# Kernel tuning notes

Hardware: AMD Instinct MI355X
Metric: run time of the kernel (lower is better)

## Reference

```python
import jax, jax.numpy as jnp
import numpy as np

B, L, ENC, D, H, HD, MLP, R = 4, 512, 512, 1024, 16, 64, 4096, 32
NUM_BUCKETS, MAX_DISTANCE = 32, 128
EPS = 1e-6
NEG = -1e10


def rmsnorm(x, scale):
    var = jnp.mean(jnp.square(x), axis=-1, keepdims=True)
    return x * jax.lax.rsqrt(var + EPS) * scale


def rel_pos_bias(table, qlen, klen):
    # T5 causal (bidirectional=False) relative position bucketing.
    ctx = jnp.arange(qlen)[:, None]
    mem = jnp.arange(klen)[None, :]
    rp = mem - ctx                      # [q, k]
    n = -jnp.minimum(rp, 0)             # distance into the past
    max_exact = NUM_BUCKETS // 2
    is_small = n < max_exact
    large = max_exact + (
        jnp.log(jnp.maximum(n, 1).astype(jnp.float32) / max_exact)
        / np.log(MAX_DISTANCE / max_exact) * (NUM_BUCKETS - max_exact)
    ).astype(jnp.int32)
    large = jnp.minimum(large, NUM_BUCKETS - 1)
    bucket = jnp.where(is_small, n, large)
    return table[bucket].transpose(2, 0, 1)[None]  # [1, h, q, k]


def lora_dense(x, W, a, b):
    # x:[B,L,d]  W:[d,e]  a:[B,d,r]  b:[B,r,e]  -> xW + (xa)b per example
    out = jnp.einsum('bld,de->ble', x, W)
    low = jnp.einsum('bld,bdr->blr', x, a)
    return out + jnp.einsum('blr,bre->ble', low, b)


def attention(xq, xkv, Wq, Wk, Wv, Wo, qa, qb, ka, kb, va, vb, oa, ob, bias):
    b, ql, _ = xq.shape
    kl = xkv.shape[1]
    q = lora_dense(xq, Wq, qa, qb).reshape(b, ql, H, HD) * (1.0 / np.sqrt(HD))
    k = lora_dense(xkv, Wk, ka, kb).reshape(b, kl, H, HD)
    v = lora_dense(xkv, Wv, va, vb).reshape(b, kl, H, HD)
    scores = jnp.einsum('bqhd,bkhd->bhqk', q, k)
    if bias is not None:
        scores = scores + bias
    probs = jax.nn.softmax(scores, axis=-1)
    ctx = jnp.einsum('bhqk,bkhd->bqhd', probs, v).reshape(b, ql, H * HD)
    return lora_dense(ctx, Wo, oa, ob)


def setup_inputs() -> dict:
    key = jax.random.key(0)
    ks = jax.random.split(key, 32)
    s = 0.02
    inp = {
        'inputs':  jax.random.normal(ks[0], (B, L, D), jnp.float32),
        'encoded': jax.random.normal(ks[1], (B, ENC, D), jnp.float32),
        'lora_qa': jax.random.normal(ks[2], (B, 2, D, R), jnp.float32) * s,
        'lora_qb': jax.random.normal(ks[3], (B, 2, R, D), jnp.float32) * s,
        'lora_ka': jax.random.normal(ks[4], (B, 2, D, R), jnp.float32) * s,
        'lora_kb': jax.random.normal(ks[5], (B, 2, R, D), jnp.float32) * s,
        'lora_va': jax.random.normal(ks[6], (B, 2, D, R), jnp.float32) * s,
        'lora_vb': jax.random.normal(ks[7], (B, 2, R, D), jnp.float32) * s,
        'lora_oa': jax.random.normal(ks[8], (B, 2, D, R), jnp.float32) * s,
        'lora_ob': jax.random.normal(ks[9], (B, 2, R, D), jnp.float32) * s,
        'rel_table': jax.random.normal(ks[10], (NUM_BUCKETS, H), jnp.float32) * s,
        'ln1': jnp.ones((D,), jnp.float32),
        'ln2': jnp.ones((D,), jnp.float32),
        'ln3': jnp.ones((D,), jnp.float32),
        'sWq': jax.random.normal(ks[11], (D, H * HD), jnp.float32) * s,
        'sWk': jax.random.normal(ks[12], (D, H * HD), jnp.float32) * s,
        'sWv': jax.random.normal(ks[13], (D, H * HD), jnp.float32) * s,
        'sWo': jax.random.normal(ks[14], (H * HD, D), jnp.float32) * s,
        'cWq': jax.random.normal(ks[15], (D, H * HD), jnp.float32) * s,
        'cWk': jax.random.normal(ks[16], (D, H * HD), jnp.float32) * s,
        'cWv': jax.random.normal(ks[17], (D, H * HD), jnp.float32) * s,
        'cWo': jax.random.normal(ks[18], (H * HD, D), jnp.float32) * s,
        'wi0': jax.random.normal(ks[19], (D, MLP), jnp.float32) * s,
        'wi1': jax.random.normal(ks[20], (D, MLP), jnp.float32) * s,
        'wo_mlp': jax.random.normal(ks[21], (MLP, D), jnp.float32) * s,
    }
    return inp


def reference(inputs, encoded, lora_qa, lora_qb, lora_ka, lora_kb, lora_va, lora_vb,
              lora_oa, lora_ob, rel_table, ln1, ln2, ln3,
              sWq, sWk, sWv, sWo, cWq, cWk, cWv, cWo, wi0, wi1, wo_mlp):
    l = inputs.shape[1]
    causal = jnp.tril(jnp.ones((l, l), dtype=bool))
    dec_bias = rel_pos_bias(rel_table, l, l) + jnp.where(causal, 0.0, NEG)[None, None]

    # --- self-attention block ---
    x = rmsnorm(inputs, ln1)
    x = attention(x, x, sWq, sWk, sWv, sWo,
                  lora_qa[:, 0], lora_qb[:, 0], lora_ka[:, 0], lora_kb[:, 0],
                  lora_va[:, 0], lora_vb[:, 0], lora_oa[:, 0], lora_ob[:, 0],
                  dec_bias)
    x = x + inputs

    # --- cross-attention block ---
    y = rmsnorm(x, ln2)
    y = attention(y, encoded, cWq, cWk, cWv, cWo,
                  lora_qa[:, 1], lora_qb[:, 1], lora_ka[:, 1], lora_kb[:, 1],
                  lora_va[:, 1], lora_vb[:, 1], lora_oa[:, 1], lora_ob[:, 1],
                  None)
    y = y + x

    # --- gated-gelu MLP block (T5 v1.1 style) ---
    lz = rmsnorm(y, ln3)
    h = jax.nn.gelu(lz @ wi0, approximate=False) * (lz @ wi1)
    z = h @ wo_mlp + y
    return z
```

## Files before the change

### kernel.cpp

```cpp
#include <hip/hip_runtime.h>
#include <math.h>


#define DEV __device__ __forceinline__

typedef __bf16 bf16x8 __attribute__((ext_vector_type(8)));
typedef float floatx4 __attribute__((ext_vector_type(4)));

typedef __attribute__((address_space(1))) void* gas_ptr;
typedef __attribute__((address_space(3))) void* las_ptr;

DEV unsigned short f2bf(float f) {
  union { float f; unsigned int u; } v; v.f = f;
  unsigned int r = v.u + 0x7fffu + ((v.u >> 16) & 1u);
  return (unsigned short)(r >> 16);
}
DEV float bf2f(unsigned short u) {
  union { unsigned int u; float f; } v; v.u = ((unsigned int)u) << 16;
  return v.f;
}

#define GLOAD_LDS16(g, l) __builtin_amdgcn_global_load_lds((gas_ptr)(g), (las_ptr)(l), 16, 0, 0)

template<int NW>
DEV void stage_tile(const char* gbase, char* lds, int nrows, int ldbytes, int wave, int lane) {
  int nchunks = nrows >> 3;
  for (int c = wave; c < nchunks; c += NW) {
    int row  = (c << 3) + (lane >> 3);
    int colb = (lane & 7) << 4;
    GLOAD_LDS16(gbase + (size_t)row * ldbytes + colb, lds + (c << 10));
  }
}

template<int NW>
DEV void stage_tile_sw(const char* gbase, char* lds, int nrows, int ldbytes, int wave, int lane) {
  int nchunks = nrows >> 3;
  int colb = (((lane & 7) ^ ((lane >> 3) & 7)) << 4);
  for (int c = wave; c < nchunks; c += NW) {
    int row = (c << 3) + (lane >> 3);
    GLOAD_LDS16(gbase + (size_t)row * ldbytes + colb, lds + (c << 10));
  }
}

template<int NW>
DEV void stage_tile256(const char* gbase, char* lds, int nrows, int ldbytes, int wave, int lane) {
  int nchunks = nrows >> 2;
  for (int c = wave; c < nchunks; c += NW) {
    int row  = (c << 2) + (lane >> 4);
    int colb = (lane & 15) << 4;
    GLOAD_LDS16(gbase + (size_t)row * ldbytes + colb, lds + (c << 10));
  }
}

template<int WM, int WN>
DEV void gemm_core(const unsigned short* A, const unsigned short* Bt, float* C,
                   int K, int lda, int ldb, int ldc, int m0, int n0,
                   char* ldsA, char* ldsB) {
  constexpr int NW = WM * WN;
  const int tid  = threadIdx.x;
  const int lane = tid & 63;
  const int wave = tid >> 6;
  const int wm   = wave % WM;
  const int wn   = wave / WM;
  const int quad = lane >> 4;
  const int l15  = lane & 15;
  const int key  = l15 & 7;

  floatx4 acc[4][4];
#pragma unroll
  for (int i = 0; i < 4; ++i)
#pragma unroll
    for (int j = 0; j < 4; ++j) acc[i][j] = (floatx4){0.f, 0.f, 0.f, 0.f};

  const char* gA = (const char*)(A + (size_t)m0 * lda);
  const char* gB = (const char*)(Bt + (size_t)n0 * ldb);

  for (int k0 = 0; k0 < K; k0 += 64) {
    stage_tile_sw<NW>(gA + (size_t)k0 * 2, ldsA, WM * 64, lda * 2, wave, lane);
    stage_tile_sw<NW>(gB + (size_t)k0 * 2, ldsB, WN * 64, ldb * 2, wave, lane);
    __syncthreads();
#pragma unroll
    for (int kk = 0; kk < 64; kk += 32) {
      bf16x8 af[4], bv[4];
      int off = (((kk >> 3) + quad) ^ key) << 4;
      const char* baseA = ldsA + (size_t)(wm * 64 + l15) * 128 + off;
      const char* baseB = ldsB + (size_t)(wn * 64 + l15) * 128 + off;
#pragma unroll
      for (int mi = 0; mi < 4; ++mi) af[mi] = *(const bf16x8*)(baseA + mi * 2048);
#pragma unroll
      for (int ni = 0; ni < 4; ++ni) bv[ni] = *(const bf16x8*)(baseB + ni * 2048);
#pragma unroll
      for (int mi = 0; mi < 4; ++mi)
#pragma unroll
        for (int ni = 0; ni < 4; ++ni)
          acc[mi][ni] = __builtin_amdgcn_mfma_f32_16x16x32_bf16(af[mi], bv[ni], acc[mi][ni], 0, 0, 0);
    }
    __syncthreads();
  }

#pragma unroll
  for (int mi = 0; mi < 4; ++mi) {
#pragma unroll
    for (int r = 0; r < 4; ++r) {
      int row = m0 + wm * 64 + mi * 16 + quad * 4 + r;
#pragma unroll
      for (int ni = 0; ni < 4; ++ni) {
        int col = n0 + wn * 64 + ni * 16 + l15;
        C[(size_t)row * ldc + col] = acc[mi][ni][r];
      }
    }
  }
}

__global__ __launch_bounds__(256) void k_gemm1s(const unsigned short* A, const unsigned short* Bt,
                                                float* Cpart, size_t pstride,
                                                int Kchunk, int lda, int ldb, int ldc) {
  __shared__ char lds[32768];
  int s = blockIdx.z;
  size_t koff = (size_t)s * Kchunk;
  gemm_core<2, 2>(A + koff, Bt + koff, Cpart + (size_t)s * pstride,
                  Kchunk, lda, ldb, ldc,
                  blockIdx.y * 128, blockIdx.x * 128, lds, lds + 16384);
}

struct GXSlice {
  const unsigned short* A0;
  const unsigned short* Aext;
  const unsigned short* B0;
  const unsigned short* Bext;
  float* C;
  size_t bextb;
  int ldc, nxa, it0, it1;
};
struct GX { GXSlice s[4]; };

__global__ __launch_bounds__(256) void k_gemmx(GX g) {
  __shared__ char lds[32768];
  char* ldsA = lds;
  char* ldsB = lds + 16384;
  GXSlice sl = g.s[blockIdx.z];
  if ((int)blockIdx.x >= sl.nxa) return;
  const int m0 = blockIdx.y * 128, n0 = blockIdx.x * 128;
  const int b = m0 >> 9;
  const int tid = threadIdx.x, lane = tid & 63, wave = tid >> 6;
  const int wm = wave & 1, wn = wave >> 1;
  const int quad = lane >> 4, l15 = lane & 15;
  const int key = l15 & 7;

  floatx4 acc[4][4];
#pragma unroll
  for (int i = 0; i < 4; ++i)
#pragma unroll
    for (int j = 0; j < 4; ++j) acc[i][j] = (floatx4){0.f, 0.f, 0.f, 0.f};

  for (int it = sl.it0; it < sl.it1; ++it) {
    if (it < 16) {
      stage_tile_sw<4>((const char*)sl.A0 + (size_t)m0 * 2048 + it * 128, ldsA, 128, 2048, wave, lane);
      stage_tile_sw<4>((const char*)sl.B0 + (size_t)n0 * 2048 + it * 128, ldsB, 128, 2048, wave, lane);
    } else {
      int eb = (it - 16) * 128;
      stage_tile_sw<4>((const char*)sl.Aext + (size_t)m0 * 256 + eb, ldsA, 128, 256, wave, lane);
      stage_tile_sw<4>((const char*)(sl.Bext + (size_t)b * sl.bextb) + (size_t)n0 * 256 + eb,
                       ldsB, 128, 256, wave, lane);
    }
    __syncthreads();
#pragma unroll
    for (int kk = 0; kk < 64; kk += 32) {
      bf16x8 af[4], bv[4];
      int off = (((kk >> 3) + quad) ^ key) << 4;
      const char* baseA = ldsA + (size_t)(wm * 64 + l15) * 128 + off;
      const char* baseB = ldsB + (size_t)(wn * 64 + l15) * 128 + off;
#pragma unroll
      for (int mi = 0; mi < 4; ++mi) af[mi] = *(const bf16x8*)(baseA + mi * 2048);
#pragma unroll
      for (int ni = 0; ni < 4; ++ni) bv[ni] = *(const bf16x8*)(baseB + ni * 2048);
#pragma unroll
      for (int mi = 0; mi < 4; ++mi)
#pragma unroll
        for (int ni = 0; ni < 4; ++ni)
          acc[mi][ni] = __builtin_amdgcn_mfma_f32_16x16x32_bf16(af[mi], bv[ni], acc[mi][ni], 0, 0, 0);
    }
    __syncthreads();
  }

#pragma unroll
  for (int mi = 0; mi < 4; ++mi) {
#pragma unroll
    for (int r = 0; r < 4; ++r) {
      int row = m0 + wm * 64 + mi * 16 + quad * 4 + r;
#pragma unroll
      for (int ni = 0; ni < 4; ++ni) {
        int col = n0 + wn * 64 + ni * 16 + l15;
        sl.C[(size_t)row * sl.ldc + col] = acc[mi][ni][r];
      }
    }
  }
}

__global__ __launch_bounds__(256) void k_qkvsum(const float* bqs, const float* bqc,
                                                unsigned short* qbf, unsigned short* kbf,
                                                unsigned short* kbf2) {
  const size_t PS = (size_t)2048 * 3072, PC = (size_t)2048 * 2048;
  int t = threadIdx.x;
  int row0 = blockIdx.x * 8;
  int zc = blockIdx.y;
  for (int j = 0; j < 8; ++j) {
    int row = row0 + j;
    int nsec = zc ? 1 : 2;
    for (int sec = 0; sec < nsec; ++sec) {
      const float* base = zc ? (bqc + (size_t)row * 2048 + sec * 1024)
                             : (bqs + (size_t)row * 3072 + sec * 1024);
      float4 a = ((const float4*)base)[t];
      float4 c = ((const float4*)(base + (zc ? PC : PS)))[t];
      float4 s; s.x = a.x + c.x; s.y = a.y + c.y; s.z = a.z + c.z; s.w = a.w + c.w;
      ushort4 o; o.x = f2bf(s.x); o.y = f2bf(s.y); o.z = f2bf(s.z); o.w = f2bf(s.w);
      unsigned short* dst = zc ? kbf2 : (sec == 0 ? qbf : kbf);
      ((ushort4*)(dst + (size_t)row * 1024))[t] = o;
    }
  }
}

__global__ __launch_bounds__(256) void k_vtrans2(const float* bqs, const float* bqc,
                                                 unsigned short* vtb, unsigned short* vtb2) {
  __shared__ float tl[64][65];
  int which = blockIdx.z;
  int z = blockIdx.y, b = z >> 4, h = z & 15;
  int k0 = blockIdx.x * 64;
  int ld = which ? 2048 : 3072;
  int voff = which ? 1024 : 2048;
  const float* src = which ? bqc : bqs;
  size_t PARTW = (size_t)2048 * ld;
  unsigned short* dst = which ? vtb2 : vtb;
  int t = threadIdx.x;
  {
    int kr = t >> 2, c0 = (t & 3) * 16;
    const float* p = src + (size_t)(b * 512 + k0 + kr) * ld + voff + h * 64 + c0;
#pragma unroll
    for (int i = 0; i < 4; ++i) {
      float4 v0 = *(const float4*)(p + i * 4);
      float4 v1 = *(const float4*)(p + PARTW + i * 4);
      tl[kr][c0 + i * 4 + 0] = v0.x + v1.x;
      tl[kr][c0 + i * 4 + 1] = v0.y + v1.y;
      tl[kr][c0 + i * 4 + 2] = v0.z + v1.z;
      tl[kr][c0 + i * 4 + 3] = v0.w + v1.w;
    }
  }
  __syncthreads();
  {
    int dw = t >> 2, kc = (t & 3) * 16;
    union { unsigned short us[16]; uint4 q[2]; } pk;
#pragma unroll
    for (int j = 0; j < 16; ++j) pk.us[j] = f2bf(tl[kc + j][dw]);
    uint4* dp = (uint4*)(dst + ((size_t)z * 64 + dw) * 512 + k0 + kc);
    dp[0] = pk.q[0]; dp[1] = pk.q[1];
  }
}

template<bool CAUSAL, bool QSUM>
__global__ __launch_bounds__(256) void k_flash(const unsigned short* qmat, const float* qparts,
                                               const unsigned short* kmat, const unsigned short* vt,
                                               const float* rb, unsigned short* ctxb) {
  __shared__ char ldsQ[8192];
  __shared__ char ldsK[16384];
  __shared__ char ldsV[16384];
  __shared__ char ldsP[16384];
  __shared__ float lrb[512];

  const size_t PART = (size_t)2048 * 1024;
  const int z = blockIdx.y, b = z >> 4, h = z & 15;
  const int q0 = blockIdx.x * 64;
  const int tid = threadIdx.x, lane = tid & 63, wave = tid >> 6;
  const int quad = lane >> 4, l15 = lane & 15;

  const unsigned short* K = kmat + (size_t)b * 512 * 1024 + h * 64;
  const unsigned short* V = vt + (size_t)z * 64 * 512;

  if (QSUM) {
#pragma unroll
    for (int rr = 0; rr < 4; ++rr) {
      int row = rr * 16 + (tid >> 4);
      int c4 = tid & 15;
      const float* src = qparts + (size_t)(q0 + row) * 1024 + h * 64 + c4 * 4;
      float4 s0 = *(const float4*)src;
      float4 s1 = *(const float4*)(src + PART);
      float4 s2 = *(const float4*)(src + 2 * PART);
      float4 s3 = *(const float4*)(src + 3 * PART);
      ushort4 o;
      o.x = f2bf(s0.x + s1.x + s2.x + s3.x);
      o.y = f2bf(s0.y + s1.y + s2.y + s3.y);
      o.z = f2bf(s0.z + s1.z + s2.z + s3.z);
      o.w = f2bf(s0.w + s1.w + s2.w + s3.w);
      *(ushort4*)(ldsQ + (size_t)row * 128 + c4 * 8) = o;
    }
  } else {
    const unsigned short* Q = qmat + (size_t)b * 512 * 1024 + h * 64;
    stage_tile<4>((const char*)(Q + (size_t)q0 * 1024), ldsQ, 64, 2048, wave, lane);
  }
  if (CAUSAL)
    for (int i = tid; i < 512; i += 256) lrb[i] = rb[h * 512 + i];

  float m_run[4], l_run[4];
  floatx4 oacc[4];
#pragma unroll
  for (int r = 0; r < 4; ++r) { m_run[r] = -1e30f; l_run[r] = 0.f; }
#pragma unroll
  for (int ni = 0; ni < 4; ++ni) oacc[ni] = (floatx4){0.f, 0.f, 0.f, 0.f};

  const int ktend = CAUSAL ? (blockIdx.x / 2 + 1) : 4;
  for (int kt = 0; kt < ktend; ++kt) {
    __syncthreads();
    stage_tile<4>((const char*)(K + (size_t)kt * 128 * 1024), ldsK, 128, 2048, wave, lane);
    stage_tile256<4>((const char*)(V + kt * 128), ldsV, 64, 1024, wave, lane);
    __syncthreads();

    floatx4 sacc[8];
#pragma unroll
    for (int ct = 0; ct < 8; ++ct) sacc[ct] = (floatx4){0.f, 0.f, 0.f, 0.f};
    const char* aBase = ldsQ + (size_t)(wave * 16 + l15) * 128 + quad * 16;
#pragma unroll
    for (int kd = 0; kd < 2; ++kd) {
      bf16x8 af = *(const bf16x8*)(aBase + kd * 64);
#pragma unroll
      for (int ct = 0; ct < 8; ++ct) {
        bf16x8 bf = *(const bf16x8*)(ldsK + (size_t)(ct * 16 + l15) * 128 + quad * 16 + kd * 64);
        sacc[ct] = __builtin_amdgcn_mfma_f32_16x16x32_bf16(af, bf, sacc[ct], 0, 0, 0);
      }
    }

    float sv[8][4];
#pragma unroll
    for (int ct = 0; ct < 8; ++ct)
#pragma unroll
      for (int r = 0; r < 4; ++r) {
        float v = sacc[ct][r] * 0.125f;
        if (CAUSAL) {
          int qq = q0 + wave * 16 + quad * 4 + r;
          int kk = kt * 128 + ct * 16 + l15;
          v = (kk <= qq) ? v + lrb[qq - kk] : -1e30f;
        }
        sv[ct][r] = v;
      }

    float mx[4];
#pragma unroll
    for (int r = 0; r < 4; ++r) {
      mx[r] = sv[0][r];
#pragma unroll
      for (int ct = 1; ct < 8; ++ct) mx[r] = fmaxf(mx[r], sv[ct][r]);
    }
#pragma unroll
    for (int o = 1; o < 16; o <<= 1)
#pragma unroll
      for (int r = 0; r < 4; ++r) mx[r] = fmaxf(mx[r], __shfl_xor(mx[r], o));

    float alpha[4], rs[4];
#pragma unroll
    for (int r = 0; r < 4; ++r) {
      float mn = fmaxf(m_run[r], mx[r]);
      alpha[r] = __expf(m_run[r] - mn);
      m_run[r] = mn;
      rs[r] = 0.f;
    }
#pragma unroll
    for (int ct = 0; ct < 8; ++ct)
#pragma unroll
      for (int r = 0; r < 4; ++r) {
        float p = __expf(sv[ct][r] - m_run[r]);
        sv[ct][r] = p;
        rs[r] += p;
      }
#pragma unroll
    for (int o = 1; o < 16; o <<= 1)
#pragma unroll
      for (int r = 0; r < 4; ++r) rs[r] += __shfl_xor(rs[r], o);
#pragma unroll
    for (int r = 0; r < 4; ++r) l_run[r] = l_run[r] * alpha[r] + rs[r];
#pragma unroll
    for (int ni = 0; ni < 4; ++ni)
#pragma unroll
      for (int r = 0; r < 4; ++r) oacc[ni][r] *= alpha[r];

#pragma unroll
    for (int ct = 0; ct < 8; ++ct)
#pragma unroll
      for (int r = 0; r < 4; ++r)
        *(unsigned short*)(ldsP + (size_t)(wave * 16 + quad * 4 + r) * 256 + (ct * 16 + l15) * 2)
            = f2bf(sv[ct][r]);
    __syncthreads();

    const char* pBase = ldsP + (size_t)(wave * 16 + l15) * 256 + quad * 16;
#pragma unroll
    for (int kk = 0; kk < 4; ++kk) {
      bf16x8 pf = *(const bf16x8*)(pBase + kk * 64);
#pragma unroll
      for (int ni = 0; ni < 4; ++ni) {
        bf16x8 vf8 = *(const bf16x8*)(ldsV + (size_t)(ni * 16 + l15) * 256 + quad * 16 + kk * 64);
        oacc[ni] = __builtin_amdgcn_mfma_f32_16x16x32_bf16(pf, vf8, oacc[ni], 0, 0, 0);
      }
    }
  }

#pragma unroll
  for (int r = 0; r < 4; ++r) {
    int q = q0 + wave * 16 + quad * 4 + r;
    float inv = 1.0f / l_run[r];
    unsigned short* dst = ctxb + ((size_t)b * 512 + q) * 1024 + h * 64;
#pragma unroll
    for (int ni = 0; ni < 4; ++ni)
      dst[ni * 16 + l15] = f2bf(oacc[ni][r] * inv);
  }
}

__global__ __launch_bounds__(512) void k_mlp(const unsigned short* A, const unsigned short* Wc,
                                             unsigned short* hbf) {
  __shared__ char lds[49152];
  char* ldsA = lds;
  char* ldsB = lds + 16384;
  const int m0 = blockIdx.y * 128;
  const int n0 = blockIdx.x * 128;
  const int tid = threadIdx.x, lane = tid & 63, wave = tid >> 6;
  const int half = wave >> 2, wl = wave & 3;
  const int wm = wl & 1, wn = wl >> 1;
  const int quad = lane >> 4, l15 = lane & 15;
  const int key = l15 & 7;

  floatx4 acc[4][4];
#pragma unroll
  for (int i = 0; i < 4; ++i)
#pragma unroll
    for (int j = 0; j < 4; ++j) acc[i][j] = (floatx4){0.f, 0.f, 0.f, 0.f};

  const char* gA = (const char*)(A + (size_t)m0 * 1024);
  const char* gB = (const char*)(Wc + (size_t)blockIdx.x * 256 * 1024);

  for (int k0 = 0; k0 < 1024; k0 += 64) {
    stage_tile_sw<8>(gA + (size_t)k0 * 2, ldsA, 128, 2048, wave, lane);
    stage_tile_sw<8>(gB + (size_t)k0 * 2, ldsB, 256, 2048, wave, lane);
    __syncthreads();
#pragma unroll
    for (int kk = 0; kk < 64; kk += 32) {
      bf16x8 af[4], bv[4];
      int off = (((kk >> 3) + quad) ^ key) << 4;
      const char* baseA = ldsA + (size_t)(wm * 64 + l15) * 128 + off;
      const char* baseB = ldsB + (size_t)(half * 128 + wn * 64 + l15) * 128 + off;
#pragma unroll
      for (int mi = 0; mi < 4; ++mi) af[mi] = *(const bf16x8*)(baseA + mi * 2048);
#pragma unroll
      for (int ni = 0; ni < 4; ++ni) bv[ni] = *(const bf16x8*)(baseB + ni * 2048);
#pragma unroll
      for (int mi = 0; mi < 4; ++mi)
#pragma unroll
        for (int ni = 0; ni < 4; ++ni)
          acc[mi][ni] = __builtin_amdgcn_mfma_f32_16x16x32_bf16(af[mi], bv[ni], acc[mi][ni], 0, 0, 0);
    }
    __syncthreads();
  }

  if (half == 1) {
#pragma unroll
    for (int mi = 0; mi < 4; ++mi)
#pragma unroll
      for (int r = 0; r < 4; ++r) {
        int row = wm * 64 + mi * 16 + quad * 4 + r;
#pragma unroll
        for (int ni = 0; ni < 4; ++ni) {
          int col = wn * 64 + ni * 16 + l15;
          *(unsigned short*)(ldsB + (size_t)row * 256 + col * 2) = f2bf(acc[mi][ni][r]);
        }
      }
  }
  __syncthreads();
  if (half == 0) {
#pragma unroll
    for (int mi = 0; mi < 4; ++mi)
#pragma unroll
      for (int r = 0; r < 4; ++r) {
        int row = wm * 64 + mi * 16 + quad * 4 + r;
#pragma unroll
        for (int ni = 0; ni < 4; ++ni) {
          int col = wn * 64 + ni * 16 + l15;
          float h1 = bf2f(*(const unsigned short*)(ldsB + (size_t)row * 256 + col * 2));
          float g = acc[mi][ni][r];
          float v = 0.5f * g * (1.0f + erff(g * 0.70710678f)) * h1;
          hbf[(size_t)(m0 + row) * 4096 + n0 + col] = f2bf(v);
        }
      }
  }
}

struct PrepArgs {
  const float* src[11];
  unsigned short* dst[11];
  int K[11], N[11], mode[11];
  int tstart[12];
  const float* encoded;
  unsigned short* encbf;
  const float* table;
  float* rb;
  unsigned short* bmdst[5];
  const float* bmsrc[5][3];
  int bmnrg[5];
  int bmstart[6];
  const float* lca[2];
  unsigned short* lowc;
  int nwt, nf2bf, nbm;
};
__global__ __launch_bounds__(256) void k_prep(PrepArgs a) {
  __shared__ char shm[49152];
  int bid = blockIdx.x;
  int t = threadIdx.x;
  if (bid < a.nwt) {
    float (*tl)[65] = (float(*)[65])shm;
    int z = 0;
    while (z < 10 && bid >= a.tstart[z + 1]) ++z;
    int tile = bid - a.tstart[z];
    int N = a.N[z], K = a.K[z], mode = a.mode[z];
    int ntn = N >> 6;
    int tn = tile % ntn, tk = tile / ntn;
    const float* src = a.src[z] + (size_t)(tk * 64) * N + tn * 64;
    unsigned short* dst = a.dst[z];
    {
      int rq = t >> 4, c4 = (t & 15) * 4;
#pragma unroll
      for (int i = 0; i < 4; ++i) {
        int r = rq + i * 16;
        float4 v = *(const float4*)(src + (size_t)r * N + c4);
        tl[r][c4] = v.x; tl[r][c4 + 1] = v.y; tl[r][c4 + 2] = v.z; tl[r][c4 + 3] = v.w;
      }
    }
    __syncthreads();
    {
      int nl = t >> 2, kseg = (t & 3) * 16;
      int n = tn * 64 + nl;
      int orow = (mode == 0) ? n : ((n >> 7) * 256 + ((mode == 2) ? 128 : 0) + (n & 127));
      union { unsigned short us[16]; uint4 q[2]; } pk;
#pragma unroll
      for (int j = 0; j < 16; ++j) pk.us[j] = f2bf(tl[kseg + j][nl]);
      uint4* dp = (uint4*)(dst + (size_t)orow * K + tk * 64 + kseg);
      dp[0] = pk.q[0]; dp[1] = pk.q[1];
    }
    return;
  }
  bid -= a.nwt;
  if (bid < a.nf2bf) {
    int i = bid * 256 + t;
    float4 v = ((const float4*)a.encoded)[i];
    ushort4 o;
    o.x = f2bf(v.x); o.y = f2bf(v.y); o.z = f2bf(v.z); o.w = f2bf(v.w);
    ((ushort4*)a.encbf)[i] = o;
    return;
  }
  bid -= a.nf2bf;
  if (bid < 32) {
    int i = bid * 256 + t;
    if (i < 16 * 512) {
      int h = i >> 9, d = i & 511;
      int bucket;
      if (d < 16) bucket = d;
      else {
        int lb = 16 + (int)(logf((float)d / 16.0f) / logf(8.0f) * 16.0f);
        bucket = lb < 31 ? lb : 31;
      }
      a.rb[i] = a.table[bucket * 16 + h];
    }
    return;
  }
  bid -= 32;
  if (bid < a.nbm) {
    int m = 0;
    while (m < 4 && bid >= a.bmstart[m + 1]) ++m;
    int idx = bid - a.bmstart[m];
    int nrg = a.bmnrg[m];
    int b = idx / nrg, rg = idx % nrg;
    int n0 = rg * 128;
    int sec = n0 >> 10;
    const float* src = a.bmsrc[m][sec] + (size_t)b * 65536;
    unsigned short* dst = a.bmdst[m] + ((size_t)b * nrg * 128 + n0) * 128;
    int n = t & 127, coff = (t >> 7) * 64;
    int ncol = (n0 & 1023) + n;
    unsigned short* drow = dst + (size_t)n * 128 + coff;
    for (int c4 = 0; c4 < 16; ++c4) {
      ushort4 o;
#pragma unroll
      for (int e = 0; e < 4; ++e) {
        int c = coff + c4 * 4 + e;
        float v = ((c >> 5) == sec) ? src[(size_t)(c & 31) * 1024 + ncol] : 0.f;
        ((unsigned short*)&o)[e] = f2bf(v);
      }
      *(ushort4*)(drow + c4 * 4) = o;
    }
    return;
  }
  bid -= a.nbm;
  {
    float* rowsF = (float*)shm;
    float* pacc = (float*)(shm + 32768);
    int row0 = bid * 8;
    int b = row0 >> 9;
    for (int j = 0; j < 8; ++j)
      ((float4*)(rowsF + j * 1024))[t] = ((const float4*)(a.encoded + (size_t)(row0 + j) * 1024))[t];
    __syncthreads();
    int r = t & 31, g = t >> 5;
    float acc[2][8];
#pragma unroll
    for (int p = 0; p < 2; ++p)
#pragma unroll
      for (int j = 0; j < 8; ++j) acc[p][j] = 0.f;
    const float* a0 = a.lca[0] + (size_t)b * 65536;
    const float* a1 = a.lca[1] + (size_t)b * 65536;
    for (int i = 0; i < 128; ++i) {
      int k = g * 128 + i;
      float ak = a0[(size_t)k * 32 + r];
      float av = a1[(size_t)k * 32 + r];
#pragma unroll
      for (int j = 0; j < 8; ++j) {
        float x = rowsF[j * 1024 + k];
        acc[0][j] += x * ak;
        acc[1][j] += x * av;
      }
    }
#pragma unroll
    for (int p = 0; p < 2; ++p)
#pragma unroll
      for (int j = 0; j < 8; ++j)
        pacc[((p * 8 + j) * 8 + g) * 32 + r] = acc[p][j];
    __syncthreads();
    for (int j = 0; j < 8; ++j) {
      if (t < 64) {
        int p = t >> 5, r2 = t & 31;
        float s = 0.f;
        for (int gg = 0; gg < 8; ++gg) s += pacc[((p * 8 + j) * 8 + gg) * 32 + r2];
        a.lowc[(size_t)(row0 + j) * 128 + p * 32 + r2] = f2bf(s);
      } else if (t < 128) {
        a.lowc[(size_t)(row0 + j) * 128 + t] = 0;
      }
    }
  }
}

__global__ __launch_bounds__(256) void k_start(const float* x, const float* sc,
                                               const float* qa, const float* ka, const float* va,
                                               unsigned short* xn, unsigned short* lowext) {
  __shared__ unsigned short lrows[8][1024];
  __shared__ float pacc[3 * 8 * 8 * 32];
  __shared__ float red[4];
  int t = threadIdx.x;
  int row0 = blockIdx.x * 8;
  int b = row0 >> 9;
  float4 s4 = ((const float4*)sc)[t];
  for (int j = 0; j < 8; ++j) {
    int row = row0 + j;
    float4 v = ((const float4*)(x + (size_t)row * 1024))[t];
    float ss = v.x * v.x + v.y * v.y + v.z * v.z + v.w * v.w;
    for (int o = 32; o; o >>= 1) ss += __shfl_down(ss, o);
    if ((t & 63) == 0) red[t >> 6] = ss;
    __syncthreads();
    float tot = red[0] + red[1] + red[2] + red[3];
    float rs = rsqrtf(tot * (1.0f / 1024.0f) + 1e-6f);
    ushort4 o;
    o.x = f2bf(v.x * rs * s4.x); o.y = f2bf(v.y * rs * s4.y);
    o.z = f2bf(v.z * rs * s4.z); o.w = f2bf(v.w * rs * s4.w);
    ((ushort4*)(xn + (size_t)row * 1024))[t] = o;
    *(ushort4*)(&lrows[j][t * 4]) = o;
    __syncthreads();
  }
  int r = t & 31, g = t >> 5;
  float acc[3][8];
#pragma unroll
  for (int p = 0; p < 3; ++p)
#pragma unroll
    for (int j = 0; j < 8; ++j) acc[p][j] = 0.f;
  const float* aq = qa + (size_t)b * 65536;
  const float* ak = ka + (size_t)b * 65536;
  const float* av = va + (size_t)b * 65536;
  for (int i = 0; i < 128; ++i) {
    int k = g * 128 + i;
    float a0 = aq[(size_t)k * 32 + r];
    float a1 = ak[(size_t)k * 32 + r];
    float a2 = av[(size_t)k * 32 + r];
#pragma unroll
    for (int j = 0; j < 8; ++j) {
      float xv = bf2f(lrows[j][k]);
      acc[0][j] += xv * a0;
      acc[1][j] += xv * a1;
      acc[2][j] += xv * a2;
    }
  }
#pragma unroll
  for (int p = 0; p < 3; ++p)
#pragma unroll
    for (int j = 0; j < 8; ++j)
      pacc[((p * 8 + j) * 8 + g) * 32 + r] = acc[p][j];
  __syncthreads();
  for (int j = 0; j < 8; ++j) {
    if (t < 96) {
      int p = t >> 5, r2 = t & 31;
      float s = 0.f;
      for (int gg = 0; gg < 8; ++gg) s += pacc[((p * 8 + j) * 8 + gg) * 32 + r2];
      lowext[(size_t)(row0 + j) * 128 + p * 32 + r2] = f2bf(s);
    } else if (t < 128) {
      lowext[(size_t)(row0 + j) * 128 + t] = 0;
    }
  }
}

template<bool LOW>
__global__ __launch_bounds__(256) void k_addbrms(const float* parts, const float* resid,
                                                 const float* sc, float* resout,
                                                 unsigned short* xn,
                                                 const float* aP, unsigned short* lowext) {
  __shared__ unsigned short lrows[8][1024];
  __shared__ float pacc[8 * 8 * 32];
  __shared__ float red[4];
  const size_t PART = (size_t)2048 * 1024;
  int t = threadIdx.x;
  int row0 = blockIdx.x * 8;
  int b = row0 >> 9;
  float4 s4 = ((const float4*)sc)[t];
  for (int j = 0; j < 8; ++j) {
    int row = row0 + j;
    const float* p0 = parts + (size_t)row * 1024;
    float4 v = ((const float4*)p0)[t];
    float4 v1 = ((const float4*)(p0 + PART))[t];
    float4 v2 = ((const float4*)(p0 + 2 * PART))[t];
    float4 v3 = ((const float4*)(p0 + 3 * PART))[t];
    float4 rv = ((const float4*)(resid + (size_t)row * 1024))[t];
    float4 s;
    s.x = v.x + v1.x + v2.x + v3.x + rv.x;
    s.y = v.y + v1.y + v2.y + v3.y + rv.y;
    s.z = v.z + v1.z + v2.z + v3.z + rv.z;
    s.w = v.w + v1.w + v2.w + v3.w + rv.w;
    ((float4*)(resout + (size_t)row * 1024))[t] = s;
    float ss = s.x * s.x + s.y * s.y + s.z * s.z + s.w * s.w;
    for (int o = 32; o; o >>= 1) ss += __shfl_down(ss, o);
    if ((t & 63) == 0) red[t >> 6] = ss;
    __syncthreads();
    float tot = red[0] + red[1] + red[2] + red[3];
    float rs = rsqrtf(tot * (1.0f / 1024.0f) + 1e-6f);
    ushort4 o;
    o.x = f2bf(s.x * rs * s4.x); o.y = f2bf(s.y * rs * s4.y);
    o.z = f2bf(s.z * rs * s4.z); o.w = f2bf(s.w * rs * s4.w);
    ((ushort4*)(xn + (size_t)row * 1024))[t] = o;
    if (LOW) *(ushort4*)(&lrows[j][t * 4]) = o;
    __syncthreads();
  }
  if (LOW) {
    int r = t & 31, g = t >> 5;
    float acc[8];
#pragma unroll
    for (int j = 0; j < 8; ++j) acc[j] = 0.f;
    const float* ap = aP + (size_t)b * 65536;
    for (int i = 0; i < 128; ++i) {
      int k = g * 128 + i;
      float a0 = ap[(size_t)k * 32 + r];
#pragma unroll
      for (int j = 0; j < 8; ++j) acc[j] += bf2f(lrows[j][k]) * a0;
    }
#pragma unroll
    for (int j = 0; j < 8; ++j) pacc[(j * 8 + g) * 32 + r] = acc[j];
    __syncthreads();
    for (int j = 0; j < 8; ++j) {
      if (t < 32) {
        float s = 0.f;
        for (int gg = 0; gg < 8; ++gg) s += pacc[(j * 8 + gg) * 32 + t];
        lowext[(size_t)(row0 + j) * 128 + t] = f2bf(s);
      } else if (t < 128) {
        lowext[(size_t)(row0 + j) * 128 + t] = 0;
      }
    }
  }
}

__global__ __launch_bounds__(256) void k_lowbf(const unsigned short* x, const float* a,
                                               unsigned short* lowext) {
  int row0 = blockIdx.x * 8;
  int b = row0 >> 9;
  int t = threadIdx.x, r = t & 31, j = t >> 5;
  int row = row0 + j;
  const bf16x8* xv = (const bf16x8*)(x + (size_t)row * 1024);
  const float* ap = a + (size_t)b * 65536;
  float s = 0.f;
  for (int kb = 0; kb < 128; ++kb) {
    bf16x8 v = xv[kb];
#pragma unroll
    for (int u = 0; u < 8; ++u)
      s += (float)v[u] * ap[(size_t)(kb * 8 + u) * 32 + r];
  }
  lowext[(size_t)row * 128 + r] = f2bf(s);
  lowext[(size_t)row * 128 + 32 + r] = 0;
  lowext[(size_t)row * 128 + 64 + r] = 0;
  lowext[(size_t)row * 128 + 96 + r] = 0;
}

__global__ void k_sum4(const float* p, size_t pstride, const float* resid, float* out) {
  int i = blockIdx.x * 256 + threadIdx.x;
  float4 a = ((const float4*)p)[i];
  float4 b = ((const float4*)(p + pstride))[i];
  float4 c = ((const float4*)(p + 2 * pstride))[i];
  float4 d = ((const float4*)(p + 3 * pstride))[i];
  float4 r = ((const float4*)resid)[i];
  float4 o;
  o.x = a.x + b.x + c.x + d.x + r.x;
  o.y = a.y + b.y + c.y + d.y + r.y;
  o.z = a.z + b.z + c.z + d.z + r.z;
  o.w = a.w + b.w + c.w + d.w + r.w;
  ((float4*)out)[i] = o;
}


extern "C" void kernel_launch(void* const* d_in, const int* in_sizes, int n_in,
                              void* d_out, int out_size, void* d_ws, size_t ws_size,
                              hipStream_t stream) {
  const float* f_inputs  = (const float*)d_in[0];
  const float* f_encoded = (const float*)d_in[1];
  const float* f_qa = (const float*)d_in[2];
  const float* f_qb = (const float*)d_in[3];
  const float* f_ka = (const float*)d_in[4];
  const float* f_kb = (const float*)d_in[5];
  const float* f_va = (const float*)d_in[6];
  const float* f_vb = (const float*)d_in[7];
  const float* f_oa = (const float*)d_in[8];
  const float* f_ob = (const float*)d_in[9];
  const float* f_table = (const float*)d_in[10];
  const float* f_ln1 = (const float*)d_in[11];
  const float* f_ln2 = (const float*)d_in[12];
  const float* f_ln3 = (const float*)d_in[13];
  const float* f_W[8] = { (const float*)d_in[14], (const float*)d_in[15],
                          (const float*)d_in[16], (const float*)d_in[17],
                          (const float*)d_in[18], (const float*)d_in[19],
                          (const float*)d_in[20], (const float*)d_in[21] };
  const float* f_wi0 = (const float*)d_in[22];
  const float* f_wi1 = (const float*)d_in[23];
  const float* f_wo  = (const float*)d_in[24];

  const size_t SEL1 = 32768;
  const size_t PART = (size_t)2048 * 1024;

  char* w = (char*)d_ws;
  size_t off = 0;
  auto alloc = [&](size_t bytes) -> char* {
    off = (off + 255) & ~(size_t)255;
    char* p = w + off;
    off += bytes;
    return p;
  };
  unsigned short* wt  = (unsigned short*)alloc((size_t)8192 * 1024 * 2);
  unsigned short* wc  = (unsigned short*)alloc((size_t)8192 * 1024 * 2);
  unsigned short* wot = (unsigned short*)alloc((size_t)1024 * 4096 * 2);
  unsigned short* encbf = (unsigned short*)alloc(2048 * 1024 * 2);
  float* rb = (float*)alloc(16 * 512 * 4);
  unsigned short* xn  = (unsigned short*)alloc(2048 * 1024 * 2);
  unsigned short* qbf = (unsigned short*)alloc(2048 * 1024 * 2);
  unsigned short* kbf = (unsigned short*)alloc(2048 * 1024 * 2);
  unsigned short* vtb = (unsigned short*)alloc((size_t)64 * 64 * 512 * 2);
  unsigned short* kbf2 = (unsigned short*)alloc(2048 * 1024 * 2);
  unsigned short* vtb2 = (unsigned short*)alloc((size_t)64 * 64 * 512 * 2);
  unsigned short* lowext_s = (unsigned short*)alloc(2048 * 128 * 2);
  unsigned short* lowext_c = (unsigned short*)alloc(2048 * 128 * 2);
  unsigned short* lowext_q = (unsigned short*)alloc(2048 * 128 * 2);
  unsigned short* lowext_o = (unsigned short*)alloc(2048 * 128 * 2);
  unsigned short* bmext_s  = (unsigned short*)alloc((size_t)4 * 3072 * 128 * 2);
  unsigned short* bmext_c  = (unsigned short*)alloc((size_t)4 * 2048 * 128 * 2);
  unsigned short* bmext_q  = (unsigned short*)alloc((size_t)4 * 1024 * 128 * 2);
  unsigned short* bmext_o  = (unsigned short*)alloc((size_t)4 * 1024 * 128 * 2);
  unsigned short* bmext_o2 = (unsigned short*)alloc((size_t)4 * 1024 * 128 * 2);
  unsigned short* ctxb = (unsigned short*)alloc(2048 * 1024 * 2);
  float* xres = (float*)alloc(2048 * 1024 * 4);
  float* yres = (float*)alloc(2048 * 1024 * 4);
  char*  big  = alloc((size_t)84 << 20);
  float* bqs  = (float*)big;
  float* bqc  = (float*)(big + ((size_t)48 << 20));
  float* op_s = (float*)big;
  float* qp_c = (float*)(big + ((size_t)32 << 20));
  float* op_c = (float*)big;
  unsigned short* hbf = (unsigned short*)big;
  float* fp   = (float*)(big + ((size_t)16 << 20));
  (void)ws_size; (void)in_sizes; (void)n_in; (void)out_size;

  PrepArgs pa;
  int ts = 0;
  for (int i = 0; i < 8; ++i) {
    pa.src[i] = f_W[i]; pa.dst[i] = wt + (size_t)i * 1024 * 1024;
    pa.K[i] = 1024; pa.N[i] = 1024; pa.mode[i] = 0;
    pa.tstart[i] = ts; ts += 256;
  }
  pa.src[8] = f_wi0; pa.dst[8] = wc; pa.K[8] = 1024; pa.N[8] = 4096; pa.mode[8] = 1;
  pa.tstart[8] = ts; ts += 1024;
  pa.src[9] = f_wi1; pa.dst[9] = wc; pa.K[9] = 1024; pa.N[9] = 4096; pa.mode[9] = 2;
  pa.tstart[9] = ts; ts += 1024;
  pa.src[10] = f_wo; pa.dst[10] = wot; pa.K[10] = 4096; pa.N[10] = 1024; pa.mode[10] = 0;
  pa.tstart[10] = ts; ts += 1024;
  pa.tstart[11] = ts;
  pa.nwt = ts;
  pa.encoded = f_encoded; pa.encbf = encbf;
  pa.table = f_table; pa.rb = rb;
  pa.nf2bf = 2048;
  pa.bmdst[0] = bmext_s;  pa.bmnrg[0] = 24;
  pa.bmsrc[0][0] = f_qb; pa.bmsrc[0][1] = f_kb; pa.bmsrc[0][2] = f_vb;
  pa.bmdst[1] = bmext_c;  pa.bmnrg[1] = 16;
  pa.bmsrc[1][0] = f_kb + SEL1; pa.bmsrc[1][1] = f_vb + SEL1; pa.bmsrc[1][2] = nullptr;
  pa.bmdst[2] = bmext_q;  pa.bmnrg[2] = 8;
  pa.bmsrc[2][0] = f_qb + SEL1; pa.bmsrc[2][1] = nullptr; pa.bmsrc[2][2] = nullptr;
  pa.bmdst[3] = bmext_o;  pa.bmnrg[3] = 8;
  pa.bmsrc[3][0] = f_ob; pa.bmsrc[3][1] = nullptr; pa.bmsrc[3][2] = nullptr;
  pa.bmdst[4] = bmext_o2; pa.bmnrg[4] = 8;
  pa.bmsrc[4][0] = f_ob + SEL1; pa.bmsrc[4][1] = nullptr; pa.bmsrc[4][2] = nullptr;
  int bs = 0;
  for (int m = 0; m < 5; ++m) { pa.bmstart[m] = bs; bs += pa.bmnrg[m] * 4; }
  pa.bmstart[5] = bs;
  pa.nbm = bs;
  pa.lca[0] = f_ka + SEL1; pa.lca[1] = f_va + SEL1;
  pa.lowc = lowext_c;
  int totblk = pa.nwt + pa.nf2bf + 32 + pa.nbm + 256;
  k_prep<<<dim3(totblk), dim3(256), 0, stream>>>(pa);

  k_start<<<dim3(256), dim3(256), 0, stream>>>(f_inputs, f_ln1, f_qa, f_ka, f_va, xn, lowext_s);

  {
    GX g;
    const size_t PS = (size_t)2048 * 3072, PC = (size_t)2048 * 2048;
    g.s[0] = { xn, lowext_s, wt, bmext_s, bqs,            (size_t)3072 * 128, 3072, 24, 0, 9 };
    g.s[1] = { xn, lowext_s, wt, bmext_s, bqs + PS,       (size_t)3072 * 128, 3072, 24, 9, 18 };
    g.s[2] = { encbf, lowext_c, wt + (size_t)5120 * 1024, bmext_c, bqc,      (size_t)2048 * 128, 2048, 16, 0, 9 };
    g.s[3] = { encbf, lowext_c, wt + (size_t)5120 * 1024, bmext_c, bqc + PC, (size_t)2048 * 128, 2048, 16, 9, 18 };
    k_gemmx<<<dim3(24, 16, 4), dim3(256), 0, stream>>>(g);
  }
  k_qkvsum<<<dim3(256, 2), dim3(256), 0, stream>>>(bqs, bqc, qbf, kbf, kbf2);
  k_vtrans2<<<dim3(8, 64, 2), dim3(256), 0, stream>>>(bqs, bqc, vtb, vtb2);

  k_flash<true, false><<<dim3(8, 64), dim3(256), 0, stream>>>(qbf, nullptr, kbf, vtb, rb, ctxb);

  k_lowbf<<<dim3(256), dim3(256), 0, stream>>>(ctxb, f_oa, lowext_o);
  {
    GX g;
    for (int s = 0; s < 4; ++s)
      g.s[s] = { ctxb, lowext_o, wt + (size_t)3072 * 1024, bmext_o, op_s + (size_t)s * PART,
                 (size_t)1024 * 128, 1024, 8, s * 18 / 4, (s + 1) * 18 / 4 };
    k_gemmx<<<dim3(8, 16, 4), dim3(256), 0, stream>>>(g);
  }
  k_addbrms<true><<<dim3(256), dim3(256), 0, stream>>>(op_s, f_inputs, f_ln2, xres, xn,
                                                       f_qa + SEL1, lowext_q);

  {
    GX g;
    for (int s = 0; s < 4; ++s)
      g.s[s] = { xn, lowext_q, wt + (size_t)4096 * 1024, bmext_q, qp_c + (size_t)s * PART,
                 (size_t)1024 * 128, 1024, 8, s * 18 / 4, (s + 1) * 18 / 4 };
    k_gemmx<<<dim3(8, 16, 4), dim3(256), 0, stream>>>(g);
  }
  k_flash<false, true><<<dim3(8, 64), dim3(256), 0, stream>>>(nullptr, qp_c, kbf2, vtb2, rb, ctxb);

  k_lowbf<<<dim3(256), dim3(256), 0, stream>>>(ctxb, f_oa + SEL1, lowext_o);
  {
    GX g;
    for (int s = 0; s < 4; ++s)
      g.s[s] = { ctxb, lowext_o, wt + (size_t)7168 * 1024, bmext_o2, op_c + (size_t)s * PART,
                 (size_t)1024 * 128, 1024, 8, s * 18 / 4, (s + 1) * 18 / 4 };
    k_gemmx<<<dim3(8, 16, 4), dim3(256), 0, stream>>>(g);
  }
  k_addbrms<false><<<dim3(256), dim3(256), 0, stream>>>(op_c, xres, f_ln3, yres, xn,
                                                        nullptr, nullptr);

  k_mlp<<<dim3(32, 16), dim3(512), 0, stream>>>(xn, wc, hbf);
  k_gemm1s<<<dim3(8, 16, 4), dim3(256), 0, stream>>>(hbf, wot, fp, PART, 1024, 4096, 4096, 1024);
  k_sum4<<<dim3(2048), dim3(256), 0, stream>>>(fp, PART, yres, (float*)d_out);
}
```

Baseline: 581.3 us.

## Swizzle flash-attention LDS tiles and split low-rank cross projection out of prep

Applies an XOR swizzle to the Q, K, V and P tiles in the flash attention kernel's shared memory. Staging, Q-sum writes, P writes and MFMA operand reads all use the same swizzled offsets, which is meant to cut LDS bank conflicts. It also moves the encoder LoRA low-rank projection out of the monolithic prep kernel into its own k_lowc kernel. That shrinks prep's shared memory from 48KB to a small padded tile, which may raise prep occupancy at the cost of an extra launch.

```diff
diff --git a/kernel.cpp b/kernel.cpp
--- a/kernel.cpp
+++ b/kernel.cpp
@@ -21,16 +21,6 @@
 }
 
 #define GLOAD_LDS16(g, l) __builtin_amdgcn_global_load_lds((gas_ptr)(g), (las_ptr)(l), 16, 0, 0)
-
-template<int NW>
-DEV void stage_tile(const char* gbase, char* lds, int nrows, int ldbytes, int wave, int lane) {
-  int nchunks = nrows >> 3;
-  for (int c = wave; c < nchunks; c += NW) {
-    int row  = (c << 3) + (lane >> 3);
-    int colb = (lane & 7) << 4;
-    GLOAD_LDS16(gbase + (size_t)row * ldbytes + colb, lds + (c << 10));
-  }
-}
 
 template<int NW>
 DEV void stage_tile_sw(const char* gbase, char* lds, int nrows, int ldbytes, int wave, int lane) {
@@ -43,11 +33,12 @@
 }
 
 template<int NW>
-DEV void stage_tile256(const char* gbase, char* lds, int nrows, int ldbytes, int wave, int lane) {
+DEV void stage_tile256_sw(const char* gbase, char* lds, int nrows, int ldbytes, int wave, int lane) {
   int nchunks = nrows >> 2;
   for (int c = wave; c < nchunks; c += NW) {
-    int row  = (c << 2) + (lane >> 4);
-    int colb = (lane & 15) << 4;
+    int row = (c << 2) + (lane >> 4);
+    int key = row & 7;
+    int colb = ((lane & 15) ^ key) << 4;
     GLOAD_LDS16(gbase + (size_t)row * ldbytes + colb, lds + (c << 10));
   }
 }
@@ -271,6 +262,7 @@
   const int q0 = blockIdx.x * 64;
   const int tid = threadIdx.x, lane = tid & 63, wave = tid >> 6;
   const int quad = lane >> 4, l15 = lane & 15;
+  const int key = l15 & 7;
 
   const unsigned short* K = kmat + (size_t)b * 512 * 1024 + h * 64;
   const unsigned short* V = vt + (size_t)z * 64 * 512;
@@ -290,11 +282,12 @@
       o.y = f2bf(s0.y + s1.y + s2.y + s3.y);
       o.z = f2bf(s0.z + s1.z + s2.z + s3.z);
       o.w = f2bf(s0.w + s1.w + s2.w + s3.w);
-      *(ushort4*)(ldsQ + (size_t)row * 128 + c4 * 8) = o;
+      int qoff = (((c4 >> 1) ^ (row & 7)) << 4) | ((c4 & 1) << 3);
+      *(ushort4*)(ldsQ + (size_t)row * 128 + qoff) = o;
     }
   } else {
     const unsigned short* Q = qmat + (size_t)b * 512 * 1024 + h * 64;
-    stage_tile<4>((const char*)(Q + (size_t)q0 * 1024), ldsQ, 64, 2048, wave, lane);
+    stage_tile_sw<4>((const char*)(Q + (size_t)q0 * 1024), ldsQ, 64, 2048, wave, lane);
   }
   if (CAUSAL)
     for (int i = tid; i < 512; i += 256) lrb[i] = rb[h * 512 + i];
@@ -309,21 +302,22 @@
   const int ktend = CAUSAL ? (blockIdx.x / 2 + 1) : 4;
   for (int kt = 0; kt < ktend; ++kt) {
     __syncthreads();
-    stage_tile<4>((const char*)(K + (size_t)kt * 128 * 1024), ldsK, 128, 2048, wave, lane);
-    stage_tile256<4>((const char*)(V + kt * 128), ldsV, 64, 1024, wave, lane);
+    stage_tile_sw<4>((const char*)(K + (size_t)kt * 128 * 1024), ldsK, 128, 2048, wave, lane);
+    stage_tile256_sw<4>((const char*)(V + kt * 128), ldsV, 64, 1024, wave, lane);
     __syncthreads();
 
     floatx4 sacc[8];
 #pragma unroll
     for (int ct = 0; ct < 8; ++ct) sacc[ct] = (floatx4){0.f, 0.f, 0.f, 0.f};
-    const char* aBase = ldsQ + (size_t)(wave * 16 + l15) * 128 + quad * 16;
+    const size_t qrow = (size_t)(wave * 16 + l15) * 128;
 #pragma unroll
     for (int kd = 0; kd < 2; ++kd) {
-      bf16x8 af = *(const bf16x8*)(aBase + kd * 64);
+      int offq = ((quad + kd * 4) ^ key) << 4;
+      bf16x8 af = *(const bf16x8*)(ldsQ + qrow + offq);
 #pragma unroll
       for (int ct = 0; ct < 8; ++ct) {
-        bf16x8 bf = *(const bf16x8*)(ldsK + (size_t)(ct * 16 + l15) * 128 + quad * 16 + kd * 64);
-        sacc[ct] = __builtin_amdgcn_mfma_f32_16x16x32_bf16(af, bf, sacc[ct], 0, 0, 0);
+        bf16x8 bfv = *(const bf16x8*)(ldsK + (size_t)(ct * 16 + l15) * 128 + offq);
+        sacc[ct] = __builtin_amdgcn_mfma_f32_16x16x32_bf16(af, bfv, sacc[ct], 0, 0, 0);
       }
     }
 
@@ -383,18 +377,22 @@
 #pragma unroll
     for (int ct = 0; ct < 8; ++ct)
 #pragma unroll
-      for (int r = 0; r < 4; ++r)
-        *(unsigned short*)(ldsP + (size_t)(wave * 16 + quad * 4 + r) * 256 + (ct * 16 + l15) * 2)
-            = f2bf(sv[ct][r]);
-    __syncthreads();
-
-    const char* pBase = ldsP + (size_t)(wave * 16 + l15) * 256 + quad * 16;
+      for (int r = 0; r < 4; ++r) {
+        int prow_w = wave * 16 + quad * 4 + r;
+        int kidx = ct * 16 + l15;
+        int pb = (((kidx >> 3) ^ (prow_w & 7)) << 4) | ((kidx & 7) << 1);
+        *(unsigned short*)(ldsP + (size_t)prow_w * 256 + pb) = f2bf(sv[ct][r]);
+      }
+    __syncthreads();
+
+    const size_t prow = (size_t)(wave * 16 + l15) * 256;
 #pragma unroll
     for (int kk = 0; kk < 4; ++kk) {
-      bf16x8 pf = *(const bf16x8*)(pBase + kk * 64);
+      int offp = ((quad + kk * 4) ^ key) << 4;
+      bf16x8 pf = *(const bf16x8*)(ldsP + prow + offp);
 #pragma unroll
       for (int ni = 0; ni < 4; ++ni) {
-        bf16x8 vf8 = *(const bf16x8*)(ldsV + (size_t)(ni * 16 + l15) * 256 + quad * 16 + kk * 64);
+        bf16x8 vf8 = *(const bf16x8*)(ldsV + (size_t)(ni * 16 + l15) * 256 + offp);
         oacc[ni] = __builtin_amdgcn_mfma_f32_16x16x32_bf16(pf, vf8, oacc[ni], 0, 0, 0);
       }
     }
@@ -501,16 +499,13 @@
   const float* bmsrc[5][3];
   int bmnrg[5];
   int bmstart[6];
-  const float* lca[2];
-  unsigned short* lowc;
   int nwt, nf2bf, nbm;
 };
 __global__ __launch_bounds__(256) void k_prep(PrepArgs a) {
-  __shared__ char shm[49152];
+  __shared__ float tl[64][65];
   int bid = blockIdx.x;
   int t = threadIdx.x;
   if (bid < a.nwt) {
-    float (*tl)[65] = (float(*)[65])shm;
     int z = 0;
     while (z < 10 && bid >= a.tstart[z + 1]) ++z;
     int tile = bid - a.tstart[z];
@@ -566,7 +561,7 @@
     return;
   }
   bid -= 32;
-  if (bid < a.nbm) {
+  {
     int m = 0;
     while (m < 4 && bid >= a.bmstart[m + 1]) ++m;
     int idx = bid - a.bmstart[m];
@@ -589,51 +584,52 @@
       }
       *(ushort4*)(drow + c4 * 4) = o;
     }
-    return;
-  }
-  bid -= a.nbm;
-  {
-    float* rowsF = (float*)shm;
-    float* pacc = (float*)(shm + 32768);
-    int row0 = bid * 8;
-    int b = row0 >> 9;
+  }
+}
+
+__global__ __launch_bounds__(256) void k_lowc(const float* encoded, const float* a0g,
+                                              const float* a1g, unsigned short* lowc) {
+  __shared__ float rowsF[8 * 1024];
+  __shared__ float pacc[2 * 8 * 8 * 32];
+  int t = threadIdx.x;
+  int row0 = blockIdx.x * 8;
+  int b = row0 >> 9;
+  for (int j = 0; j < 8; ++j)
+    ((float4*)(rowsF + j * 1024))[t] = ((const float4*)(encoded + (size_t)(row0 + j) * 1024))[t];
+  __syncthreads();
+  int r = t & 31, g = t >> 5;
+  float acc[2][8];
+#pragma unroll
+  for (int p = 0; p < 2; ++p)
+#pragma unroll
+    for (int j = 0; j < 8; ++j) acc[p][j] = 0.f;
+  const float* a0 = a0g + (size_t)b * 65536;
+  const float* a1 = a1g + (size_t)b * 65536;
+  for (int i = 0; i < 128; ++i) {
+    int k = g * 128 + i;
+    float ak = a0[(size_t)k * 32 + r];
+    float av = a1[(size_t)k * 32 + r];
+#pragma unroll
+    for (int j = 0; j < 8; ++j) {
+      float x = rowsF[j * 1024 + k];
+      acc[0][j] += x * ak;
+      acc[1][j] += x * av;
+    }
+  }
+#pragma unroll
+  for (int p = 0; p < 2; ++p)
+#pragma unroll
     for (int j = 0; j < 8; ++j)
-      ((float4*)(rowsF + j * 1024))[t] = ((const float4*)(a.encoded + (size_t)(row0 + j) * 1024))[t];
-    __syncthreads();
-    int r = t & 31, g = t >> 5;
-    float acc[2][8];
-#pragma unroll
-    for (int p = 0; p < 2; ++p)
-#pragma unroll
-      for (int j = 0; j < 8; ++j) acc[p][j] = 0.f;
-    const float* a0 = a.lca[0] + (size_t)b * 65536;
-    const float* a1 = a.lca[1] + (size_t)b * 65536;
-    for (int i = 0; i < 128; ++i) {
-      int k = g * 128 + i;
-      float ak = a0[(size_t)k * 32 + r];
-      float av = a1[(size_t)k * 32 + r];
-#pragma unroll
-      for (int j = 0; j < 8; ++j) {
-        float x = rowsF[j * 1024 + k];
-        acc[0][j] += x * ak;
-        acc[1][j] += x * av;
-      }
-    }
-#pragma unroll
-    for (int p = 0; p < 2; ++p)
-#pragma unroll
-      for (int j = 0; j < 8; ++j)
-        pacc[((p * 8 + j) * 8 + g) * 32 + r] = acc[p][j];
-    __syncthreads();
-    for (int j = 0; j < 8; ++j) {
-      if (t < 64) {
-        int p = t >> 5, r2 = t & 31;
-        float s = 0.f;
-        for (int gg = 0; gg < 8; ++gg) s += pacc[((p * 8 + j) * 8 + gg) * 32 + r2];
-        a.lowc[(size_t)(row0 + j) * 128 + p * 32 + r2] = f2bf(s);
-      } else if (t < 128) {
-        a.lowc[(size_t)(row0 + j) * 128 + t] = 0;
-      }
+      pacc[((p * 8 + j) * 8 + g) * 32 + r] = acc[p][j];
+  __syncthreads();
+  for (int j = 0; j < 8; ++j) {
+    if (t < 64) {
+      int p = t >> 5, r2 = t & 31;
+      float s = 0.f;
+      for (int gg = 0; gg < 8; ++gg) s += pacc[((p * 8 + j) * 8 + gg) * 32 + r2];
+      lowc[(size_t)(row0 + j) * 128 + p * 32 + r2] = f2bf(s);
+    } else if (t < 128) {
+      lowc[(size_t)(row0 + j) * 128 + t] = 0;
     }
   }
 }
@@ -909,10 +905,9 @@
   for (int m = 0; m < 5; ++m) { pa.bmstart[m] = bs; bs += pa.bmnrg[m] * 4; }
   pa.bmstart[5] = bs;
   pa.nbm = bs;
-  pa.lca[0] = f_ka + SEL1; pa.lca[1] = f_va + SEL1;
-  pa.lowc = lowext_c;
-  int totblk = pa.nwt + pa.nf2bf + 32 + pa.nbm + 256;
+  int totblk = pa.nwt + pa.nf2bf + 32 + pa.nbm;
   k_prep<<<dim3(totblk), dim3(256), 0, stream>>>(pa);
+  k_lowc<<<dim3(256), dim3(256), 0, stream>>>(f_encoded, f_ka + SEL1, f_va + SEL1, lowext_c);
 
   k_start<<<dim3(256), dim3(256), 0, stream>>>(f_inputs, f_ln1, f_qa, f_ka, f_va, xn, lowext_s);
 
```

Result: no change. 592.7 us (+2.0%).
